# Kernel tuning notes

Hardware: AMD Instinct MI355X
Metric: run time of the kernel (lower is better)

The kernel has to match this reference:

```python
import jax, jax.numpy as jnp
import numpy as np

B, T, D_MODEL, H, DK = 2, 1024, 1024, 16, 64
ADJ_TOPK, PHASE_TOPK, N_STEPS = 128, 128, 4


def _sparse_softmax(scores, k):
    # top-k per row, softmax over the kept entries, zeros elsewhere
    vals, idx = jax.lax.top_k(scores, k)            # (B,h,T,k)
    w = jax.nn.softmax(vals, axis=-1)
    b, h, t, _ = scores.shape
    bi = jnp.arange(b)[:, None, None, None]
    hi = jnp.arange(h)[None, :, None, None]
    ti = jnp.arange(t)[None, None, :, None]
    return jnp.zeros_like(scores).at[bi, hi, ti, idx].set(w)


def _heads(y):
    return y.reshape(B, T, H, DK).transpose(0, 2, 1, 3)  # (B,h,T,d_k)


def setup_inputs() -> dict:
    key = jax.random.key(0)
    ks = jax.random.split(key, 8)
    s = 0.02
    return {
        "x": jax.random.normal(ks[0], (B, T, D_MODEL), jnp.float32),
        "W_Q": jax.random.normal(ks[1], (D_MODEL, D_MODEL), jnp.float32) * s,
        "W_K": jax.random.normal(ks[2], (D_MODEL, D_MODEL), jnp.float32) * s,
        "W_re": jax.random.normal(ks[3], (D_MODEL, D_MODEL), jnp.float32) * s,
        "W_im": jax.random.normal(ks[4], (D_MODEL, D_MODEL), jnp.float32) * s,
        "W_V": jax.random.normal(ks[5], (D_MODEL, D_MODEL), jnp.float32) * s,
        "W_O": jax.random.normal(ks[6], (D_MODEL, D_MODEL), jnp.float32) * s,
        "logit_lam": jnp.float32(0.0),   # sigmoid -> lam=0.5
        "log_alpha": jnp.float32(-3.0),  # matches nn.Parameter init
    }


def reference(x, W_Q, W_K, W_re, W_im, W_V, W_O, logit_lam, log_alpha):
    # --- AdjacencyBuilder: A = sparse_softmax(QK^T/sqrt(dk)) ---
    Q = _heads(x @ W_Q.T)
    K = _heads(x @ W_K.T)
    scores = jnp.einsum('bhtd,bhsd->bhts', Q, K) / np.sqrt(DK).astype(np.float32)
    A = _sparse_softmax(scores, ADJ_TOPK)          # (B,h,T,T)

    # --- PhaseEncoding: D = W_re x + i W_im x (kept as real/imag pair) ---
    Dr = _heads(x @ W_re.T)
    Di = _heads(x @ W_im.T)
    D0r, D0i = Dr, Di

    # --- TopologyPropagation: D <- (1-lam) D + lam A D, n_steps times ---
    lam = jax.nn.sigmoid(logit_lam)
    for _ in range(N_STEPS):
        Dr = (1.0 - lam) * Dr + lam * jnp.einsum('bhts,bhsd->bhtd', A, Dr)
        Di = (1.0 - lam) * Di + lam * jnp.einsum('bhts,bhsd->bhtd', A, Di)
    alpha = jax.nn.sigmoid(log_alpha)
    Dr = Dr + alpha * D0r
    Di = Di + alpha * D0i

    # --- phase sync attention: Re(D_i . conj(D_j)) on unit-normalized D ---
    norm = jnp.maximum(jnp.sqrt(jnp.sum(Dr * Dr + Di * Di, axis=-1, keepdims=True)), 1e-6)
    Ur, Ui = Dr / norm, Di / norm
    phase_sim = (jnp.einsum('bhtd,bhsd->bhts', Ur, Ur)
                 + jnp.einsum('bhtd,bhsd->bhts', Ui, Ui)) * np.sqrt(2.0 * DK).astype(np.float32)
    phase_attn = _sparse_softmax(phase_sim, PHASE_TOPK)

    # --- weighted V sum + output projection ---
    V = _heads(x @ W_V.T)
    out = jnp.einsum('bhts,bhsd->bhtd', phase_attn, V)
    out = out.transpose(0, 2, 1, 3).reshape(B, T, D_MODEL)
    return out @ W_O.T, phase_attn
```

## Files before the change

kernel.cpp:

```cpp
#include <hip/hip_runtime.h>
#include <cstdint>
#include <cstddef>

#define B_  2
#define T_  1024
#define DM  1024
#define H_  16
#define DK_ 64
#define TOPK 128

typedef unsigned short ushort_t;
typedef __attribute__((ext_vector_type(8))) short short8;
typedef __attribute__((ext_vector_type(8))) unsigned short u16x8;
typedef __attribute__((ext_vector_type(4))) float f32x4;

__device__ __forceinline__ unsigned fkey16(unsigned b) {
  return (b & 0x8000u) ? (0xffffu & ~b) : (b | 0x8000u);
}

__device__ __forceinline__ ushort_t f2bf(float f) {
  unsigned u = __float_as_uint(f);
  return (ushort_t)((u + 0x7fffu + ((u >> 16) & 1u)) >> 16);
}
__device__ __forceinline__ float bf2f(ushort_t u) {
  return __uint_as_float((unsigned)u << 16);
}

__device__ __forceinline__ void gload_lds16(const ushort_t* g, ushort_t* l) {
  __builtin_amdgcn_global_load_lds(
      (const __attribute__((address_space(1))) unsigned int*)(const void*)g,
      (__attribute__((address_space(3))) unsigned int*)(void*)l, 16, 0, 0);
}

__global__ __launch_bounds__(256) void cast6_kernel(
    const float* __restrict__ x, const float* __restrict__ wq,
    const float* __restrict__ wk, const float* __restrict__ wre,
    const float* __restrict__ wim, const float* __restrict__ wv,
    ushort_t* __restrict__ xb, ushort_t* __restrict__ w5b) {
  int z = blockIdx.y;
  const float* src; ushort_t* dst; int n4;
  switch (z) {
    case 0: src = x;   dst = xb;                 n4 = 524288; break;
    case 1: src = wq;  dst = w5b;                n4 = 262144; break;
    case 2: src = wk;  dst = w5b + 1048576;      n4 = 262144; break;
    case 3: src = wre; dst = w5b + 2097152;      n4 = 262144; break;
    case 4: src = wim; dst = w5b + 3145728;      n4 = 262144; break;
    default: src = wv; dst = w5b + 4194304;      n4 = 262144; break;
  }
  int i = blockIdx.x * 256 + threadIdx.x;
  if (i < n4) {
    float4 v = ((const float4*)src)[i];
    ushort4 o;
    o.x = f2bf(v.x); o.y = f2bf(v.y); o.z = f2bf(v.z); o.w = f2bf(v.w);
    ((ushort4*)dst)[i] = o;
  }
}

__global__ __launch_bounds__(256) void cast_bf16_kernel(
    const float* __restrict__ in, ushort_t* __restrict__ out, int n4) {
  int i = blockIdx.x * 256 + threadIdx.x;
  if (i < n4) {
    float4 v = ((const float4*)in)[i];
    ushort4 o;
    o.x = f2bf(v.x); o.y = f2bf(v.y); o.z = f2bf(v.z); o.w = f2bf(v.w);
    ((ushort4*)out)[i] = o;
  }
}

template<int KDIM>
__device__ __forceinline__ void gemm_core(
    const ushort_t* __restrict__ Ab, const ushort_t* __restrict__ Bb,
    ushort_t* ldsA, ushort_t* ldsB, int tid, f32x4 acc[4][4]) {
  const int lane = tid & 63, wid = tid >> 6;
  const int wr = (wid >> 1) * 64, wc = (wid & 1) * 64;
  const int l15 = lane & 15, l4 = lane >> 4;
  for (int k0 = 0; k0 < KDIM; k0 += 64) {
    #pragma unroll
    for (int i = 0; i < 4; ++i) {
      int cid = tid + 256 * i;
      int row = cid >> 3, slot = cid & 7;
      int gc = slot ^ (row & 7);
      gload_lds16(&Ab[(size_t)row * KDIM + k0 + gc * 8], &ldsA[cid * 8]);
      gload_lds16(&Bb[(size_t)row * KDIM + k0 + gc * 8], &ldsB[cid * 8]);
    }
    __syncthreads();
    #pragma unroll
    for (int ks = 0; ks < 2; ++ks) {
      short8 af[4], bfr[4];
      #pragma unroll
      for (int m = 0; m < 4; ++m) {
        int r = wr + m * 16 + l15;
        int c = ks * 4 + l4;
        af[m] = *(const short8*)&ldsA[r * 64 + (c ^ (r & 7)) * 8];
      }
      #pragma unroll
      for (int n = 0; n < 4; ++n) {
        int r = wc + n * 16 + l15;
        int c = ks * 4 + l4;
        bfr[n] = *(const short8*)&ldsB[r * 64 + (c ^ (r & 7)) * 8];
      }
      #pragma unroll
      for (int m = 0; m < 4; ++m)
        #pragma unroll
        for (int n = 0; n < 4; ++n)
          acc[m][n] = __builtin_amdgcn_mfma_f32_16x16x32_bf16(
              af[m], bfr[n], acc[m][n], 0, 0, 0);
    }
    __syncthreads();
  }
}

__global__ __launch_bounds__(256) void proj5_mfma(
    const ushort_t* __restrict__ xb, const ushort_t* __restrict__ wb,
    ushort_t* __restrict__ qh_b, ushort_t* __restrict__ kh_b,
    ushort_t* __restrict__ dt0, ushort_t* __restrict__ vt_b) {
  __shared__ ushort_t ldsA[128 * 64];
  __shared__ ushort_t ldsB[128 * 64];
  int tid = threadIdx.x, z = blockIdx.z;
  const ushort_t* W = wb + (size_t)z * (DM * DM);
  f32x4 acc[4][4];
  #pragma unroll
  for (int m = 0; m < 4; ++m)
    #pragma unroll
    for (int n = 0; n < 4; ++n) acc[m][n] = (f32x4){0.f, 0.f, 0.f, 0.f};
  gemm_core<DM>(xb + (size_t)blockIdx.y * 128 * DM,
                W + (size_t)blockIdx.x * 128 * DM, ldsA, ldsB, tid, acc);
  const int lane = tid & 63, wid = tid >> 6;
  int row0 = blockIdx.y * 128 + (wid >> 1) * 64 + (lane >> 4) * 4;
  int col0 = blockIdx.x * 128 + (wid & 1) * 64 + (lane & 15);
  #pragma unroll
  for (int m = 0; m < 4; ++m)
    #pragma unroll
    for (int n = 0; n < 4; ++n)
      #pragma unroll
      for (int j = 0; j < 4; ++j) {
        int nr = row0 + m * 16 + j;
        int mc = col0 + n * 16;
        int b = nr >> 10, t = nr & 1023, h = mc >> 6, d = mc & 63;
        int head = b * H_ + h;
        float v = acc[m][n][j];
        if (z == 0) {
          qh_b[((size_t)head * T_ + t) * DK_ + d] = f2bf(v);
        } else if (z == 1) {
          kh_b[((size_t)head * T_ + t) * DK_ + d] = f2bf(v);
        } else if (z == 4) {
          vt_b[(size_t)head * 65536 + (size_t)d * 1024 + t] = f2bf(v);
        } else {
          int ddofs = (z == 3) ? 64 : 0;
          dt0[(size_t)head * 131072 + (size_t)(d + ddofs) * 1024 + t] = f2bf(v);
        }
      }
}

template<int KDIM, bool BF16OUT>
__global__ __launch_bounds__(256) void score_mfma(
    const ushort_t* __restrict__ A, const ushort_t* __restrict__ Bm,
    void* __restrict__ Sout, float scale) {
  __shared__ ushort_t ldsA[128 * 64];
  __shared__ ushort_t ldsB[128 * 64];
  int tid = threadIdx.x, z = blockIdx.z;
  f32x4 acc[4][4];
  #pragma unroll
  for (int m = 0; m < 4; ++m)
    #pragma unroll
    for (int n = 0; n < 4; ++n) acc[m][n] = (f32x4){0.f, 0.f, 0.f, 0.f};
  gemm_core<KDIM>(A + (size_t)z * T_ * KDIM + (size_t)blockIdx.y * 128 * KDIM,
                  Bm + (size_t)z * T_ * KDIM + (size_t)blockIdx.x * 128 * KDIM,
                  ldsA, ldsB, tid, acc);
  const int lane = tid & 63, wid = tid >> 6;
  int row0 = blockIdx.y * 128 + (wid >> 1) * 64 + (lane >> 4) * 4;
  int col0 = blockIdx.x * 128 + (wid & 1) * 64 + (lane & 15);
  if (BF16OUT) {
    ushort_t* Sz = (ushort_t*)Sout + (size_t)z * T_ * T_;
    #pragma unroll
    for (int m = 0; m < 4; ++m)
      #pragma unroll
      for (int n = 0; n < 4; ++n)
        #pragma unroll
        for (int j = 0; j < 4; ++j)
          Sz[(size_t)(row0 + m * 16 + j) * T_ + col0 + n * 16] =
              f2bf(acc[m][n][j] * scale);
  } else {
    float* Sz = (float*)Sout + (size_t)z * T_ * T_;
    #pragma unroll
    for (int m = 0; m < 4; ++m)
      #pragma unroll
      for (int n = 0; n < 4; ++n)
        #pragma unroll
        for (int j = 0; j < 4; ++j)
          Sz[(size_t)(row0 + m * 16 + j) * T_ + col0 + n * 16] =
              acc[m][n][j] * scale;
  }
}

__global__ __launch_bounds__(256) void prop_mfma(
    const ushort_t* __restrict__ Ab, const ushort_t* __restrict__ Dsrc,
    ushort_t* __restrict__ Ddst, const float* __restrict__ logit_lam) {
  __shared__ ushort_t ldsA[64 * 64];
  __shared__ ushort_t ldsB[128 * 64];
  int tid = threadIdx.x, hz = blockIdx.y;
  const int lane = tid & 63, wid = tid >> 6;
  const int wr = wid >> 1, wc = wid & 1;
  const int l15 = lane & 15, l4 = lane >> 4;
  const ushort_t* Ah = Ab + (size_t)hz * 1048576 + (size_t)blockIdx.x * 64 * 1024;
  const ushort_t* Dh = Dsrc + (size_t)hz * 131072;
  f32x4 acc[2][4];
  #pragma unroll
  for (int m = 0; m < 2; ++m)
    #pragma unroll
    for (int n = 0; n < 4; ++n) acc[m][n] = (f32x4){0.f, 0.f, 0.f, 0.f};
  for (int k0 = 0; k0 < 1024; k0 += 64) {
    {
      int cid = tid;
      int rowc = cid >> 3, slot = cid & 7;
      int gc = slot ^ (rowc & 7);
      gload_lds16(&Ah[(size_t)rowc * 1024 + k0 + gc * 8], &ldsA[cid * 8]);
      cid = tid + 256;
      rowc = cid >> 3; slot = cid & 7;
      gc = slot ^ (rowc & 7);
      gload_lds16(&Ah[(size_t)rowc * 1024 + k0 + gc * 8], &ldsA[cid * 8]);
    }
    #pragma unroll
    for (int i = 0; i < 4; ++i) {
      int cid = tid + 256 * i;
      int rowc = cid >> 3, slot = cid & 7;
      int gc = slot ^ (rowc & 7);
      gload_lds16(&Dh[(size_t)rowc * 1024 + k0 + gc * 8], &ldsB[cid * 8]);
    }
    __syncthreads();
    #pragma unroll
    for (int ks = 0; ks < 2; ++ks) {
      short8 af[2], bfr[4];
      #pragma unroll
      for (int m = 0; m < 2; ++m) {
        int r = wr * 32 + m * 16 + l15;
        int c = ks * 4 + l4;
        af[m] = *(const short8*)&ldsA[r * 64 + (c ^ (r & 7)) * 8];
      }
      #pragma unroll
      for (int n = 0; n < 4; ++n) {
        int r = wc * 64 + n * 16 + l15;
        int c = ks * 4 + l4;
        bfr[n] = *(const short8*)&ldsB[r * 64 + (c ^ (r & 7)) * 8];
      }
      #pragma unroll
      for (int m = 0; m < 2; ++m)
        #pragma unroll
        for (int n = 0; n < 4; ++n)
          acc[m][n] = __builtin_amdgcn_mfma_f32_16x16x32_bf16(
              af[m], bfr[n], acc[m][n], 0, 0, 0);
    }
    __syncthreads();
  }
  float lam = 1.f / (1.f + __expf(-logit_lam[0]));
  ushort_t* Dd = Ddst + (size_t)hz * 131072;
  #pragma unroll
  for (int m = 0; m < 2; ++m)
    #pragma unroll
    for (int n = 0; n < 4; ++n)
      #pragma unroll
      for (int j = 0; j < 4; ++j) {
        int t = blockIdx.x * 64 + wr * 32 + m * 16 + l4 * 4 + j;
        int dd = wc * 64 + n * 16 + l15;
        size_t o = (size_t)dd * 1024 + t;
        float oldv = bf2f(Dh[o]);
        Dd[o] = f2bf((1.f - lam) * oldv + lam * acc[m][n][j]);
      }
}

template<int MODE>
__global__ __launch_bounds__(256) void topk16_kernel(
    ushort_t* __restrict__ Sb, float* __restrict__ denseOut) {
  const int tid = threadIdx.x;
  const int lane = tid & 63, wv = tid >> 6;
  const int row = blockIdx.x * 4 + wv;
  ushort_t* Srow = Sb + (size_t)row * 1024;

  float scr[2][8];
  unsigned kk[2][8];
  #pragma unroll
  for (int g = 0; g < 2; ++g) {
    u16x8 v = *(const u16x8*)&Srow[g * 512 + lane * 8];
    #pragma unroll
    for (int e = 0; e < 8; ++e) {
      scr[g][e] = bf2f(v[e]);
      kk[g][e] = fkey16((unsigned)v[e]);
    }
  }

  unsigned prefix = 0, r = TOPK;
  #pragma unroll
  for (int b = 15; b >= 0; --b) {
    unsigned want = (prefix << 1) | 1u;
    unsigned cnt = 0;
    #pragma unroll
    for (int g = 0; g < 2; ++g)
      #pragma unroll
      for (int e = 0; e < 8; ++e)
        cnt += (unsigned)__popcll(__ballot((kk[g][e] >> b) == want));
    if (cnt >= r) prefix = want;
    else { prefix <<= 1; r -= cnt; }
  }
  const unsigned thr = prefix;

  float mx = -3.402823466e38f;
  #pragma unroll
  for (int g = 0; g < 2; ++g)
    #pragma unroll
    for (int e = 0; e < 8; ++e) mx = fmaxf(mx, scr[g][e]);
  #pragma unroll
  for (int off = 1; off < 64; off <<= 1) mx = fmaxf(mx, __shfl_xor(mx, off));

  const unsigned long long below = (1ull << lane) - 1ull;
  unsigned cum = 0;
  float w[2][8];
  float ps = 0.f;
  #pragma unroll
  for (int g = 0; g < 2; ++g) {
    unsigned long long bal[8];
    #pragma unroll
    for (int e = 0; e < 8; ++e) bal[e] = __ballot(kk[g][e] == thr);
    unsigned rb = cum;
    #pragma unroll
    for (int e = 0; e < 8; ++e) rb += (unsigned)__popcll(bal[e] & below);
    unsigned ownPrior = 0;
    #pragma unroll
    for (int e = 0; e < 8; ++e) {
      bool eq = (kk[g][e] == thr);
      bool sel = (kk[g][e] > thr) || (eq && (rb + ownPrior) < r);
      ownPrior += eq ? 1u : 0u;
      float ex = sel ? __expf(scr[g][e] - mx) : 0.f;
      w[g][e] = ex;
      ps += ex;
    }
    #pragma unroll
    for (int e = 0; e < 8; ++e) cum += (unsigned)__popcll(bal[e]);
  }
  float pss = ps;
  #pragma unroll
  for (int off = 1; off < 64; off <<= 1) pss += __shfl_xor(pss, off);
  const float inv = 1.f / pss;

  if (MODE == 0) {
    float* Drow = denseOut + (size_t)row * 1024;
    #pragma unroll
    for (int g = 0; g < 2; ++g) {
      *(float4*)&Drow[g * 512 + lane * 8] =
          make_float4(w[g][0] * inv, w[g][1] * inv, w[g][2] * inv, w[g][3] * inv);
      *(float4*)&Drow[g * 512 + lane * 8 + 4] =
          make_float4(w[g][4] * inv, w[g][5] * inv, w[g][6] * inv, w[g][7] * inv);
    }
  }
  #pragma unroll
  for (int g = 0; g < 2; ++g) {
    u16x8 o;
    #pragma unroll
    for (int e = 0; e < 8; ++e) o[e] = f2bf(w[g][e] * inv);
    *(u16x8*)&Srow[g * 512 + lane * 8] = o;
  }
}

__global__ __launch_bounds__(256) void finalize_kernel(
    const ushort_t* __restrict__ Dt, const ushort_t* __restrict__ Dt0,
    ushort_t* __restrict__ P, const float* __restrict__ log_alpha) {
  __shared__ float lds[64][129];
  __shared__ float red[4][64];
  __shared__ float nrmi[64];
  int tid = threadIdx.x;
  int hz = blockIdx.y;
  int t0 = blockIdx.x * 64;
  size_t base = (size_t)hz * 131072 + t0;
  float alpha = 1.f / (1.f + __expf(-log_alpha[0]));
  #pragma unroll
  for (int i = 0; i < 32; ++i) {
    int eid = tid + i * 256;
    int dd = eid >> 6, t = eid & 63;
    size_t o = base + (size_t)dd * 1024 + t;
    lds[t][dd] = bf2f(Dt[o]) + alpha * bf2f(Dt0[o]);
  }
  __syncthreads();
  int t = tid & 63, q = tid >> 6;
  float s = 0.f;
  #pragma unroll
  for (int k = 0; k < 32; ++k) {
    float v = lds[t][q * 32 + k];
    s += v * v;
  }
  red[q][t] = s;
  __syncthreads();
  if (tid < 64) {
    float tot = red[0][tid] + red[1][tid] + red[2][tid] + red[3][tid];
    nrmi[tid] = 1.f / fmaxf(sqrtf(tot), 1e-6f);
  }
  __syncthreads();
  #pragma unroll
  for (int i = 0; i < 32; ++i) {
    int eid = tid + i * 256;
    int dd = eid & 127, tt = eid >> 7;
    P[((size_t)hz * 1024 + t0 + tt) * 128 + dd] = f2bf(lds[tt][dd] * nrmi[tt]);
  }
}

__global__ __launch_bounds__(256) void attnv_mfma(
    const ushort_t* __restrict__ Wb, const ushort_t* __restrict__ Vt,
    ushort_t* __restrict__ attn_b) {
  __shared__ ushort_t ldsA[64 * 64];
  __shared__ ushort_t ldsB[64 * 64];
  int tid = threadIdx.x, hz = blockIdx.y;
  const int lane = tid & 63, wid = tid >> 6;
  const int wr = wid >> 1, wc = wid & 1;
  const int l15 = lane & 15, l4 = lane >> 4;
  const ushort_t* Wh = Wb + (size_t)hz * 1048576 + (size_t)blockIdx.x * 64 * 1024;
  const ushort_t* Vh = Vt + (size_t)hz * 65536;
  f32x4 acc[2][2];
  #pragma unroll
  for (int m = 0; m < 2; ++m)
    #pragma unroll
    for (int n = 0; n < 2; ++n) acc[m][n] = (f32x4){0.f, 0.f, 0.f, 0.f};
  for (int k0 = 0; k0 < 1024; k0 += 64) {
    #pragma unroll
    for (int i = 0; i < 2; ++i) {
      int cid = tid + 256 * i;
      int rowc = cid >> 3, slot = cid & 7;
      int gc = slot ^ (rowc & 7);
      gload_lds16(&Wh[(size_t)rowc * 1024 + k0 + gc * 8], &ldsA[cid * 8]);
    }
    #pragma unroll
    for (int i = 0; i < 2; ++i) {
      int cid = tid + 256 * i;
      int rowc = cid >> 3, slot = cid & 7;
      int gc = slot ^ (rowc & 7);
      gload_lds16(&Vh[(size_t)rowc * 1024 + k0 + gc * 8], &ldsB[cid * 8]);
    }
    __syncthreads();
    #pragma unroll
    for (int ks = 0; ks < 2; ++ks) {
      short8 af[2], bfr[2];
      #pragma unroll
      for (int m = 0; m < 2; ++m) {
        int r = wr * 32 + m * 16 + l15;
        int c = ks * 4 + l4;
        af[m] = *(const short8*)&ldsA[r * 64 + (c ^ (r & 7)) * 8];
      }
      #pragma unroll
      for (int n = 0; n < 2; ++n) {
        int r = wc * 32 + n * 16 + l15;
        int c = ks * 4 + l4;
        bfr[n] = *(const short8*)&ldsB[r * 64 + (c ^ (r & 7)) * 8];
      }
      #pragma unroll
      for (int m = 0; m < 2; ++m)
        #pragma unroll
        for (int n = 0; n < 2; ++n)
          acc[m][n] = __builtin_amdgcn_mfma_f32_16x16x32_bf16(
              af[m], bfr[n], acc[m][n], 0, 0, 0);
    }
    __syncthreads();
  }
  int b = hz >> 4, h = hz & 15;
  #pragma unroll
  for (int m = 0; m < 2; ++m)
    #pragma unroll
    for (int n = 0; n < 2; ++n)
      #pragma unroll
      for (int j = 0; j < 4; ++j) {
        int t = blockIdx.x * 64 + wr * 32 + m * 16 + l4 * 4 + j;
        int d = wc * 32 + n * 16 + l15;
        attn_b[((size_t)(b * T_ + t)) * DM + h * DK_ + d] = f2bf(acc[m][n][j]);
      }
}

extern "C" void kernel_launch(void* const* d_in, const int* in_sizes, int n_in,
                              void* d_out, int out_size, void* d_ws, size_t ws_size,
                              hipStream_t stream) {
  (void)in_sizes; (void)n_in; (void)out_size; (void)ws_size;
  const float* x         = (const float*)d_in[0];
  const float* wq        = (const float*)d_in[1];
  const float* wk        = (const float*)d_in[2];
  const float* wre       = (const float*)d_in[3];
  const float* wim       = (const float*)d_in[4];
  const float* wv        = (const float*)d_in[5];
  const float* wo        = (const float*)d_in[6];
  const float* logit_lam = (const float*)d_in[7];
  const float* log_alpha = (const float*)d_in[8];

  float* out   = (float*)d_out;
  float* dense = out + (size_t)B_ * T_ * DM;
  ushort_t* w5_b = (ushort_t*)dense;

  char* ws = (char*)d_ws;
  const size_t MB = (size_t)1 << 20;
  ushort_t* A_b  = (ushort_t*)(ws + 0 * MB);
  ushort_t* S2_b = A_b;
  ushort_t* dt0  = (ushort_t*)(ws + 64 * MB);
  ushort_t* dtA  = (ushort_t*)(ws + 72 * MB);
  ushort_t* P_b  = dtA;
  ushort_t* dtB  = (ushort_t*)(ws + 80 * MB);
  ushort_t* vt_b = (ushort_t*)(ws + 88 * MB);
  ushort_t* xb   = (ushort_t*)(ws + 92 * MB);
  ushort_t* attn_b = xb;
  ushort_t* qh_b = (ushort_t*)(ws + 96 * MB);
  ushort_t* wo_b = qh_b;
  ushort_t* kh_b = (ushort_t*)(ws + 100 * MB);

  const int rows = B_ * H_ * T_;

  cast6_kernel<<<dim3(2048, 6), 256, 0, stream>>>(
      x, wq, wk, wre, wim, wv, xb, w5_b);

  proj5_mfma<<<dim3(8, 16, 5), 256, 0, stream>>>(
      xb, w5_b, qh_b, kh_b, dt0, vt_b);

  score_mfma<64, true><<<dim3(8, 8, 32), 256, 0, stream>>>(
      qh_b, kh_b, A_b, 0.125f);
  cast_bf16_kernel<<<1024, 256, 0, stream>>>(wo, wo_b, DM * DM / 4);
  topk16_kernel<1><<<rows / 4, 256, 0, stream>>>(A_b, nullptr);

  prop_mfma<<<dim3(16, 32), 256, 0, stream>>>(A_b, dt0, dtA, logit_lam);
  prop_mfma<<<dim3(16, 32), 256, 0, stream>>>(A_b, dtA, dtB, logit_lam);
  prop_mfma<<<dim3(16, 32), 256, 0, stream>>>(A_b, dtB, dtA, logit_lam);
  prop_mfma<<<dim3(16, 32), 256, 0, stream>>>(A_b, dtA, dtB, logit_lam);

  finalize_kernel<<<dim3(16, 32), 256, 0, stream>>>(dtB, dt0, P_b, log_alpha);

  score_mfma<128, true><<<dim3(8, 8, 32), 256, 0, stream>>>(
      P_b, P_b, S2_b, 11.3137085f);
  topk16_kernel<0><<<rows / 4, 256, 0, stream>>>(S2_b, dense);

  attnv_mfma<<<dim3(16, 32), 256, 0, stream>>>(S2_b, vt_b, attn_b);
  score_mfma<DM, false><<<dim3(8, 16, 1), 256, 0, stream>>>(
      attn_b, wo_b, out, 1.0f);
}
```

Baseline: 378.3 us.

## Fuse final propagation with normalize, remap blocks across XCDs, retile output projection

```diff
diff --git a/kernel.cpp b/kernel.cpp
--- a/kernel.cpp
+++ b/kernel.cpp
@@ -116,18 +116,20 @@
     ushort_t* __restrict__ dt0, ushort_t* __restrict__ vt_b) {
   __shared__ ushort_t ldsA[128 * 64];
   __shared__ ushort_t ldsB[128 * 64];
-  int tid = threadIdx.x, z = blockIdx.z;
+  int tid = threadIdx.x;
+  int orig = (blockIdx.x & 7) * 80 + (blockIdx.x >> 3);
+  int bx = orig & 7, by = (orig >> 3) & 15, z = orig >> 7;
   const ushort_t* W = wb + (size_t)z * (DM * DM);
   f32x4 acc[4][4];
   #pragma unroll
   for (int m = 0; m < 4; ++m)
     #pragma unroll
     for (int n = 0; n < 4; ++n) acc[m][n] = (f32x4){0.f, 0.f, 0.f, 0.f};
-  gemm_core<DM>(xb + (size_t)blockIdx.y * 128 * DM,
-                W + (size_t)blockIdx.x * 128 * DM, ldsA, ldsB, tid, acc);
-  const int lane = tid & 63, wid = tid >> 6;
-  int row0 = blockIdx.y * 128 + (wid >> 1) * 64 + (lane >> 4) * 4;
-  int col0 = blockIdx.x * 128 + (wid & 1) * 64 + (lane & 15);
+  gemm_core<DM>(xb + (size_t)by * 128 * DM,
+                W + (size_t)bx * 128 * DM, ldsA, ldsB, tid, acc);
+  const int lane = tid & 63, wid = tid >> 6;
+  int row0 = by * 128 + (wid >> 1) * 64 + (lane >> 4) * 4;
+  int col0 = bx * 128 + (wid & 1) * 64 + (lane & 15);
   #pragma unroll
   for (int m = 0; m < 4; ++m)
     #pragma unroll
@@ -152,44 +154,82 @@
       }
 }
 
-template<int KDIM, bool BF16OUT>
+template<int KDIM>
 __global__ __launch_bounds__(256) void score_mfma(
     const ushort_t* __restrict__ A, const ushort_t* __restrict__ Bm,
-    void* __restrict__ Sout, float scale) {
+    ushort_t* __restrict__ Sout, float scale) {
   __shared__ ushort_t ldsA[128 * 64];
   __shared__ ushort_t ldsB[128 * 64];
-  int tid = threadIdx.x, z = blockIdx.z;
+  int tid = threadIdx.x;
+  int orig = (blockIdx.x & 7) * 256 + (blockIdx.x >> 3);
+  int bx = orig & 7, by = (orig >> 3) & 7, z = orig >> 6;
   f32x4 acc[4][4];
   #pragma unroll
   for (int m = 0; m < 4; ++m)
     #pragma unroll
     for (int n = 0; n < 4; ++n) acc[m][n] = (f32x4){0.f, 0.f, 0.f, 0.f};
-  gemm_core<KDIM>(A + (size_t)z * T_ * KDIM + (size_t)blockIdx.y * 128 * KDIM,
-                  Bm + (size_t)z * T_ * KDIM + (size_t)blockIdx.x * 128 * KDIM,
+  gemm_core<KDIM>(A + (size_t)z * T_ * KDIM + (size_t)by * 128 * KDIM,
+                  Bm + (size_t)z * T_ * KDIM + (size_t)bx * 128 * KDIM,
                   ldsA, ldsB, tid, acc);
   const int lane = tid & 63, wid = tid >> 6;
-  int row0 = blockIdx.y * 128 + (wid >> 1) * 64 + (lane >> 4) * 4;
-  int col0 = blockIdx.x * 128 + (wid & 1) * 64 + (lane & 15);
-  if (BF16OUT) {
-    ushort_t* Sz = (ushort_t*)Sout + (size_t)z * T_ * T_;
-    #pragma unroll
-    for (int m = 0; m < 4; ++m)
-      #pragma unroll
-      for (int n = 0; n < 4; ++n)
+  int row0 = by * 128 + (wid >> 1) * 64 + (lane >> 4) * 4;
+  int col0 = bx * 128 + (wid & 1) * 64 + (lane & 15);
+  ushort_t* Sz = Sout + (size_t)z * T_ * T_;
+  #pragma unroll
+  for (int m = 0; m < 4; ++m)
+    #pragma unroll
+    for (int n = 0; n < 4; ++n)
+      #pragma unroll
+      for (int j = 0; j < 4; ++j)
+        Sz[(size_t)(row0 + m * 16 + j) * T_ + col0 + n * 16] =
+            f2bf(acc[m][n][j] * scale);
+}
+
+__device__ __forceinline__ void mfma_64x128_loop(
+    const ushort_t* __restrict__ Ah, const ushort_t* __restrict__ Bh,
+    ushort_t* ldsA, ushort_t* ldsB, int tid, f32x4 acc[2][4]) {
+  const int lane = tid & 63, wid = tid >> 6;
+  const int wr = wid >> 1, wc = wid & 1;
+  const int l15 = lane & 15, l4 = lane >> 4;
+  for (int k0 = 0; k0 < 1024; k0 += 64) {
+    #pragma unroll
+    for (int i = 0; i < 2; ++i) {
+      int cid = tid + 256 * i;
+      int rowc = cid >> 3, slot = cid & 7;
+      int gc = slot ^ (rowc & 7);
+      gload_lds16(&Ah[(size_t)rowc * 1024 + k0 + gc * 8], &ldsA[cid * 8]);
+    }
+    #pragma unroll
+    for (int i = 0; i < 4; ++i) {
+      int cid = tid + 256 * i;
+      int rowc = cid >> 3, slot = cid & 7;
+      int gc = slot ^ (rowc & 7);
+      gload_lds16(&Bh[(size_t)rowc * 1024 + k0 + gc * 8], &ldsB[cid * 8]);
+    }
+    __syncthreads();
+    #pragma unroll
+    for (int ks = 0; ks < 2; ++ks) {
+      short8 af[2], bfr[4];
+      #pragma unroll
+      for (int m = 0; m < 2; ++m) {
+        int r = wr * 32 + m * 16 + l15;
+        int c = ks * 4 + l4;
+        af[m] = *(const short8*)&ldsA[r * 64 + (c ^ (r & 7)) * 8];
+      }
+      #pragma unroll
+      for (int n = 0; n < 4; ++n) {
+        int r = wc * 64 + n * 16 + l15;
+        int c = ks * 4 + l4;
+        bfr[n] = *(const short8*)&ldsB[r * 64 + (c ^ (r & 7)) * 8];
+      }
+      #pragma unroll
+      for (int m = 0; m < 2; ++m)
         #pragma unroll
-        for (int j = 0; j < 4; ++j)
-          Sz[(size_t)(row0 + m * 16 + j) * T_ + col0 + n * 16] =
-              f2bf(acc[m][n][j] * scale);
-  } else {
-    float* Sz = (float*)Sout + (size_t)z * T_ * T_;
-    #pragma unroll
-    for (int m = 0; m < 4; ++m)
-      #pragma unroll
-      for (int n = 0; n < 4; ++n)
-        #pragma unroll
-        for (int j = 0; j < 4; ++j)
-          Sz[(size_t)(row0 + m * 16 + j) * T_ + col0 + n * 16] =
-              acc[m][n][j] * scale;
+        for (int n = 0; n < 4; ++n)
+          acc[m][n] = __builtin_amdgcn_mfma_f32_16x16x32_bf16(
+              af[m], bfr[n], acc[m][n], 0, 0, 0);
+    }
+    __syncthreads();
   }
 }
 
@@ -198,60 +238,20 @@
     ushort_t* __restrict__ Ddst, const float* __restrict__ logit_lam) {
   __shared__ ushort_t ldsA[64 * 64];
   __shared__ ushort_t ldsB[128 * 64];
-  int tid = threadIdx.x, hz = blockIdx.y;
+  int tid = threadIdx.x;
+  int orig = (blockIdx.x & 7) * 64 + (blockIdx.x >> 3);
+  int bx = orig & 15, hz = orig >> 4;
   const int lane = tid & 63, wid = tid >> 6;
   const int wr = wid >> 1, wc = wid & 1;
   const int l15 = lane & 15, l4 = lane >> 4;
-  const ushort_t* Ah = Ab + (size_t)hz * 1048576 + (size_t)blockIdx.x * 64 * 1024;
   const ushort_t* Dh = Dsrc + (size_t)hz * 131072;
   f32x4 acc[2][4];
   #pragma unroll
   for (int m = 0; m < 2; ++m)
     #pragma unroll
     for (int n = 0; n < 4; ++n) acc[m][n] = (f32x4){0.f, 0.f, 0.f, 0.f};
-  for (int k0 = 0; k0 < 1024; k0 += 64) {
-    {
-      int cid = tid;
-      int rowc = cid >> 3, slot = cid & 7;
-      int gc = slot ^ (rowc & 7);
-      gload_lds16(&Ah[(size_t)rowc * 1024 + k0 + gc * 8], &ldsA[cid * 8]);
-      cid = tid + 256;
-      rowc = cid >> 3; slot = cid & 7;
-      gc = slot ^ (rowc & 7);
-      gload_lds16(&Ah[(size_t)rowc * 1024 + k0 + gc * 8], &ldsA[cid * 8]);
-    }
-    #pragma unroll
-    for (int i = 0; i < 4; ++i) {
-      int cid = tid + 256 * i;
-      int rowc = cid >> 3, slot = cid & 7;
-      int gc = slot ^ (rowc & 7);
-      gload_lds16(&Dh[(size_t)rowc * 1024 + k0 + gc * 8], &ldsB[cid * 8]);
-    }
-    __syncthreads();
-    #pragma unroll
-    for (int ks = 0; ks < 2; ++ks) {
-      short8 af[2], bfr[4];
-      #pragma unroll
-      for (int m = 0; m < 2; ++m) {
-        int r = wr * 32 + m * 16 + l15;
-        int c = ks * 4 + l4;
-        af[m] = *(const short8*)&ldsA[r * 64 + (c ^ (r & 7)) * 8];
-      }
-      #pragma unroll
-      for (int n = 0; n < 4; ++n) {
-        int r = wc * 64 + n * 16 + l15;
-        int c = ks * 4 + l4;
-        bfr[n] = *(const short8*)&ldsB[r * 64 + (c ^ (r & 7)) * 8];
-      }
-      #pragma unroll
-      for (int m = 0; m < 2; ++m)
-        #pragma unroll
-        for (int n = 0; n < 4; ++n)
-          acc[m][n] = __builtin_amdgcn_mfma_f32_16x16x32_bf16(
-              af[m], bfr[n], acc[m][n], 0, 0, 0);
-    }
-    __syncthreads();
-  }
+  mfma_64x128_loop(Ab + (size_t)hz * 1048576 + (size_t)bx * 64 * 1024,
+                   Dh, ldsA, ldsB, tid, acc);
   float lam = 1.f / (1.f + __expf(-logit_lam[0]));
   ushort_t* Dd = Ddst + (size_t)hz * 131072;
   #pragma unroll
@@ -260,12 +260,81 @@
     for (int n = 0; n < 4; ++n)
       #pragma unroll
       for (int j = 0; j < 4; ++j) {
-        int t = blockIdx.x * 64 + wr * 32 + m * 16 + l4 * 4 + j;
+        int t = bx * 64 + wr * 32 + m * 16 + l4 * 4 + j;
         int dd = wc * 64 + n * 16 + l15;
         size_t o = (size_t)dd * 1024 + t;
         float oldv = bf2f(Dh[o]);
         Dd[o] = f2bf((1.f - lam) * oldv + lam * acc[m][n][j]);
       }
+}
+
+__global__ __launch_bounds__(256) void prop_final_mfma(
+    const ushort_t* __restrict__ Ab, const ushort_t* __restrict__ Dsrc,
+    const ushort_t* __restrict__ Dt0, ushort_t* __restrict__ P,
+    const float* __restrict__ logit_lam, const float* __restrict__ log_alpha) {
+  __shared__ ushort_t ldsA[64 * 64];
+  __shared__ ushort_t ldsB[128 * 64];
+  __shared__ float sums[4][2][4][4];
+  int tid = threadIdx.x;
+  int orig = (blockIdx.x & 7) * 64 + (blockIdx.x >> 3);
+  int bx = orig & 15, hz = orig >> 4;
+  const int lane = tid & 63, wid = tid >> 6;
+  const int wr = wid >> 1, wc = wid & 1;
+  const int l15 = lane & 15, l4 = lane >> 4;
+  const ushort_t* Dh = Dsrc + (size_t)hz * 131072;
+  f32x4 acc[2][4];
+  #pragma unroll
+  for (int m = 0; m < 2; ++m)
+    #pragma unroll
+    for (int n = 0; n < 4; ++n) acc[m][n] = (f32x4){0.f, 0.f, 0.f, 0.f};
+  mfma_64x128_loop(Ab + (size_t)hz * 1048576 + (size_t)bx * 64 * 1024,
+                   Dh, ldsA, ldsB, tid, acc);
+  float lam = 1.f / (1.f + __expf(-logit_lam[0]));
+  float alpha = 1.f / (1.f + __expf(-log_alpha[0]));
+  const ushort_t* D0h = Dt0 + (size_t)hz * 131072;
+  float F[2][4][4];
+  float ssp[2][4];
+  #pragma unroll
+  for (int m = 0; m < 2; ++m)
+    #pragma unroll
+    for (int j = 0; j < 4; ++j) {
+      int t = bx * 64 + wr * 32 + m * 16 + l4 * 4 + j;
+      float s = 0.f;
+      #pragma unroll
+      for (int n = 0; n < 4; ++n) {
+        int dd = wc * 64 + n * 16 + l15;
+        size_t o = (size_t)dd * 1024 + t;
+        float f = (1.f - lam) * bf2f(Dh[o]) + lam * acc[m][n][j] +
+                  alpha * bf2f(D0h[o]);
+        F[m][n][j] = f;
+        s += f * f;
+      }
+      #pragma unroll
+      for (int off = 1; off < 16; off <<= 1) s += __shfl_xor(s, off);
+      ssp[m][j] = s;
+    }
+  if (l15 == 0) {
+    #pragma unroll
+    for (int m = 0; m < 2; ++m)
+      #pragma unroll
+      for (int j = 0; j < 4; ++j)
+        sums[wid][m][j][l4] = ssp[m][j];
+  }
+  __syncthreads();
+  ushort_t* Ph = P + (size_t)hz * 1024 * 128;
+  #pragma unroll
+  for (int m = 0; m < 2; ++m)
+    #pragma unroll
+    for (int j = 0; j < 4; ++j) {
+      float tot = sums[wid][m][j][l4] + sums[wid ^ 1][m][j][l4];
+      float ni = 1.f / fmaxf(sqrtf(tot), 1e-6f);
+      int t = bx * 64 + wr * 32 + m * 16 + l4 * 4 + j;
+      #pragma unroll
+      for (int n = 0; n < 4; ++n) {
+        int dd = wc * 64 + n * 16 + l15;
+        Ph[(size_t)t * 128 + dd] = f2bf(F[m][n][j] * ni);
+      }
+    }
 }
 
 template<int MODE>
@@ -360,57 +429,18 @@
   }
 }
 
-__global__ __launch_bounds__(256) void finalize_kernel(
-    const ushort_t* __restrict__ Dt, const ushort_t* __restrict__ Dt0,
-    ushort_t* __restrict__ P, const float* __restrict__ log_alpha) {
-  __shared__ float lds[64][129];
-  __shared__ float red[4][64];
-  __shared__ float nrmi[64];
-  int tid = threadIdx.x;
-  int hz = blockIdx.y;
-  int t0 = blockIdx.x * 64;
-  size_t base = (size_t)hz * 131072 + t0;
-  float alpha = 1.f / (1.f + __expf(-log_alpha[0]));
-  #pragma unroll
-  for (int i = 0; i < 32; ++i) {
-    int eid = tid + i * 256;
-    int dd = eid >> 6, t = eid & 63;
-    size_t o = base + (size_t)dd * 1024 + t;
-    lds[t][dd] = bf2f(Dt[o]) + alpha * bf2f(Dt0[o]);
-  }
-  __syncthreads();
-  int t = tid & 63, q = tid >> 6;
-  float s = 0.f;
-  #pragma unroll
-  for (int k = 0; k < 32; ++k) {
-    float v = lds[t][q * 32 + k];
-    s += v * v;
-  }
-  red[q][t] = s;
-  __syncthreads();
-  if (tid < 64) {
-    float tot = red[0][tid] + red[1][tid] + red[2][tid] + red[3][tid];
-    nrmi[tid] = 1.f / fmaxf(sqrtf(tot), 1e-6f);
-  }
-  __syncthreads();
-  #pragma unroll
-  for (int i = 0; i < 32; ++i) {
-    int eid = tid + i * 256;
-    int dd = eid & 127, tt = eid >> 7;
-    P[((size_t)hz * 1024 + t0 + tt) * 128 + dd] = f2bf(lds[tt][dd] * nrmi[tt]);
-  }
-}
-
 __global__ __launch_bounds__(256) void attnv_mfma(
     const ushort_t* __restrict__ Wb, const ushort_t* __restrict__ Vt,
     ushort_t* __restrict__ attn_b) {
   __shared__ ushort_t ldsA[64 * 64];
   __shared__ ushort_t ldsB[64 * 64];
-  int tid = threadIdx.x, hz = blockIdx.y;
+  int tid = threadIdx.x;
+  int orig = (blockIdx.x & 7) * 64 + (blockIdx.x >> 3);
+  int bx = orig & 15, hz = orig >> 4;
   const int lane = tid & 63, wid = tid >> 6;
   const int wr = wid >> 1, wc = wid & 1;
   const int l15 = lane & 15, l4 = lane >> 4;
-  const ushort_t* Wh = Wb + (size_t)hz * 1048576 + (size_t)blockIdx.x * 64 * 1024;
+  const ushort_t* Wh = Wb + (size_t)hz * 1048576 + (size_t)bx * 64 * 1024;
   const ushort_t* Vh = Vt + (size_t)hz * 65536;
   f32x4 acc[2][2];
   #pragma unroll
@@ -464,9 +494,39 @@
     for (int n = 0; n < 2; ++n)
       #pragma unroll
       for (int j = 0; j < 4; ++j) {
-        int t = blockIdx.x * 64 + wr * 32 + m * 16 + l4 * 4 + j;
+        int t = bx * 64 + wr * 32 + m * 16 + l4 * 4 + j;
         int d = wc * 32 + n * 16 + l15;
         attn_b[((size_t)(b * T_ + t)) * DM + h * DK_ + d] = f2bf(acc[m][n][j]);
+      }
+}
+
+__global__ __launch_bounds__(256) void outproj_mfma(
+    const ushort_t* __restrict__ A, const ushort_t* __restrict__ Wo,
+    float* __restrict__ out) {
+  __shared__ ushort_t ldsA[64 * 64];
+  __shared__ ushort_t ldsB[128 * 64];
+  int tid = threadIdx.x;
+  int orig = (blockIdx.x & 7) * 32 + (blockIdx.x >> 3);
+  int bx = orig & 7, by = orig >> 3;
+  const int lane = tid & 63, wid = tid >> 6;
+  const int wr = wid >> 1, wc = wid & 1;
+  const int l15 = lane & 15, l4 = lane >> 4;
+  f32x4 acc[2][4];
+  #pragma unroll
+  for (int m = 0; m < 2; ++m)
+    #pragma unroll
+    for (int n = 0; n < 4; ++n) acc[m][n] = (f32x4){0.f, 0.f, 0.f, 0.f};
+  mfma_64x128_loop(A + (size_t)by * 64 * 1024,
+                   Wo + (size_t)bx * 128 * 1024, ldsA, ldsB, tid, acc);
+  #pragma unroll
+  for (int m = 0; m < 2; ++m)
+    #pragma unroll
+    for (int n = 0; n < 4; ++n)
+      #pragma unroll
+      for (int j = 0; j < 4; ++j) {
+        int r = by * 64 + wr * 32 + m * 16 + l4 * 4 + j;
+        int c = bx * 128 + wc * 64 + n * 16 + l15;
+        out[(size_t)r * 1024 + c] = acc[m][n][j];
       }
 }
 
@@ -494,8 +554,8 @@
   ushort_t* S2_b = A_b;
   ushort_t* dt0  = (ushort_t*)(ws + 64 * MB);
   ushort_t* dtA  = (ushort_t*)(ws + 72 * MB);
-  ushort_t* P_b  = dtA;
   ushort_t* dtB  = (ushort_t*)(ws + 80 * MB);
+  ushort_t* P_b  = dtB;
   ushort_t* vt_b = (ushort_t*)(ws + 88 * MB);
   ushort_t* xb   = (ushort_t*)(ws + 92 * MB);
   ushort_t* attn_b = xb;
@@ -508,26 +568,21 @@
   cast6_kernel<<<dim3(2048, 6), 256, 0, stream>>>(
       x, wq, wk, wre, wim, wv, xb, w5_b);
 
-  proj5_mfma<<<dim3(8, 16, 5), 256, 0, stream>>>(
-      xb, w5_b, qh_b, kh_b, dt0, vt_b);
-
-  score_mfma<64, true><<<dim3(8, 8, 32), 256, 0, stream>>>(
-      qh_b, kh_b, A_b, 0.125f);
+  proj5_mfma<<<640, 256, 0, stream>>>(xb, w5_b, qh_b, kh_b, dt0, vt_b);
+
+  score_mfma<64><<<2048, 256, 0, stream>>>(qh_b, kh_b, A_b, 0.125f);
   cast_bf16_kernel<<<1024, 256, 0, stream>>>(wo, wo_b, DM * DM / 4);
   topk16_kernel<1><<<rows / 4, 256, 0, stream>>>(A_b, nullptr);
 
-  prop_mfma<<<dim3(16, 32), 256, 0, stream>>>(A_b, dt0, dtA, logit_lam);
-  prop_mfma<<<dim3(16, 32), 256, 0, stream>>>(A_b, dtA, dtB, logit_lam);
-  prop_mfma<<<dim3(16, 32), 256, 0, stream>>>(A_b, dtB, dtA, logit_lam);
-  prop_mfma<<<dim3(16, 32), 256, 0, stream>>>(A_b, dtA, dtB, logit_lam);
-
-  finalize_kernel<<<dim3(16, 32), 256, 0, stream>>>(dtB, dt0, P_b, log_alpha);
-
-  score_mfma<128, true><<<dim3(8, 8, 32), 256, 0, stream>>>(
-      P_b, P_b, S2_b, 11.3137085f);
+  prop_mfma<<<512, 256, 0, stream>>>(A_b, dt0, dtA, logit_lam);
+  prop_mfma<<<512, 256, 0, stream>>>(A_b, dtA, dtB, logit_lam);
+  prop_mfma<<<512, 256, 0, stream>>>(A_b, dtB, dtA, logit_lam);
+  prop_final_mfma<<<512, 256, 0, stream>>>(A_b, dtA, dt0, P_b,
+                                           logit_lam, log_alpha);
+
+  score_mfma<128><<<2048, 256, 0, stream>>>(P_b, P_b, S2_b, 11.3137085f);
   topk16_kernel<0><<<rows / 4, 256, 0, stream>>>(S2_b, dense);
 
-  attnv_mfma<<<dim3(16, 32), 256, 0, stream>>>(S2_b, vt_b, attn_b);
-  score_mfma<DM, false><<<dim3(8, 16, 1), 256, 0, stream>>>(
-      attn_b, wo_b, out, 1.0f);
-}
+  attnv_mfma<<<512, 256, 0, stream>>>(S2_b, vt_b, attn_b);
+  outproj_mfma<<<256, 256, 0, stream>>>(attn_b, wo_b, out);
+}
```

Result: faster. 342.7 us (-9.4%).
